# Performance work log

Measured on AMD Instinct MI355X. Metric: run time of the kernel, lower is better.

## Reference

```python
import jax, jax.numpy as jnp
import numpy as np

B, S, D, H = 4, 2048, 1024, 64  # batch, chunk_size, token_emb_dim, head_size

def setup_inputs() -> dict:
    key = jax.random.key(0)
    ks = jax.random.split(key, 6)
    sc = 0.02
    return {
        "x": jax.random.normal(ks[0], (B, S, D), dtype=jnp.float32),
        "Wq": jax.random.normal(ks[1], (D, H), dtype=jnp.float32) * sc,
        "Wk": jax.random.normal(ks[2], (D, H), dtype=jnp.float32) * sc,
        "Wv": jax.random.normal(ks[3], (D, H), dtype=jnp.float32) * sc,
        "Wproj": jax.random.normal(ks[4], (D, D), dtype=jnp.float32) * sc,
        "bproj": jax.random.normal(ks[5], (D,), dtype=jnp.float32) * sc,
        "n_heads": 16,
    }

def reference(x, Wq, Wk, Wv, Wproj, bproj, n_heads):
    # NOTE: the original torch module reuses ONE head instance n_heads times,
    # so every head produces the identical output. Compute once, tile.
    q = jnp.einsum('bsd,dh->bsh', x, Wq)
    k = jnp.einsum('bsd,dh->bsh', x, Wk)
    v = jnp.einsum('bsd,dh->bsh', x, Wv)
    scores = jnp.einsum('bqh,bkh->bqk', q, k) * (H ** -0.5)
    causal = jnp.tril(jnp.ones((S, S), dtype=bool))
    scores = jnp.where(causal[None, :, :], scores, -jnp.inf)
    attn = jax.nn.softmax(scores, axis=-1)
    ctx = jnp.einsum('bqk,bkh->bqh', attn, v)       # [B,S,H]
    out = jnp.tile(ctx, (1, 1, n_heads))            # concat of identical heads -> [B,S,D]
    return jnp.einsum('bsd,de->bse', out, Wproj) + bproj
```

## Files before the change

### kernel.cpp

```cpp
#include <hip/hip_runtime.h>
#include <hip/hip_bf16.h>
#include <math.h>

namespace {

constexpr int B = 4, S = 2048, D = 1024, H = 64, NH = 16;
constexpr int BS = B * S;
constexpr float SCALE2 = 0.125f * 1.4426950408889634f;
constexpr float M0 = 8.0f;

constexpr int AUNITS_PB = 272;
constexpr int AUNITS = AUNITS_PB * 4;

using f32x4 = __attribute__((ext_vector_type(4))) float;
using short8b = __attribute__((ext_vector_type(8))) short;

__device__ inline ushort f2bf(float f) {
    __hip_bfloat16 h = __float2bfloat16(f);
    return *reinterpret_cast<ushort*>(&h);
}
__device__ inline float bf2f(ushort u) {
    __hip_bfloat16 h = *reinterpret_cast<__hip_bfloat16*>(&u);
    return __bfloat162float(h);
}
__device__ inline int cum_units(int J) {
    return (J & 1) ? ((J + 1) * (J + 1) / 4) : (J * J / 4 + J / 2);
}

__global__ __launch_bounds__(256) void prep_kernel(const float* __restrict__ Wq,
                                                   const float* __restrict__ Wk,
                                                   const float* __restrict__ Wv,
                                                   const float* __restrict__ Wproj,
                                                   ushort* __restrict__ Wt,
                                                   ushort* __restrict__ Wpet) {
    const int bid = blockIdx.x;
    const int tid = threadIdx.x;
    if (bid < 768) {
        const int idx = bid * 256 + tid;
        const int n = idx >> 10, k = idx & 1023;
        const float* __restrict__ W = (n < 64) ? Wq : (n < 128) ? Wk : Wv;
        Wt[idx] = f2bf(W[k * 64 + (n & 63)]);
    } else {
        const int idx = (bid - 768) * 256 + tid;
        const int e = idx & 1023, h = idx >> 10;
        float s = 0.f;
#pragma unroll
        for (int t = 0; t < NH; ++t) s += Wproj[(t * H + h) * D + e];
        Wpet[e * 64 + h] = f2bf(s);
    }
}

__global__ __launch_bounds__(256) void qkv6_kernel(const float* __restrict__ x,
                                                   const ushort* __restrict__ Wt,
                                                   ushort* __restrict__ qb,
                                                   ushort* __restrict__ kb,
                                                   ushort* __restrict__ vb) {
    __shared__ ushort xs[16 * 128];
    __shared__ ushort wsm[192 * 128];
    const int tid = threadIdx.x;
    const int lane = tid & 63;
    const int li = lane & 15, lg = lane >> 4;
    const int wn = tid >> 6;
    const int row0 = blockIdx.x * 16;

    f32x4 acc[3];
#pragma unroll
    for (int t = 0; t < 3; ++t) acc[t] = (f32x4){0.f, 0.f, 0.f, 0.f};

    const int xrow = tid >> 4;
    const int xc4 = (tid & 15) * 4;

    const char* xsb = reinterpret_cast<const char*>(xs);
    const char* wsb = reinterpret_cast<const char*>(wsm);

    for (int k0 = 0; k0 < 1024; k0 += 128) {
        __syncthreads();
#pragma unroll
        for (int hh = 0; hh < 2; ++hh) {
            const float4 f = *reinterpret_cast<const float4*>(
                x + (size_t)(row0 + xrow) * 1024 + k0 + hh * 64 + xc4);
            ushort u[4] = {f2bf(f.x), f2bf(f.y), f2bf(f.z), f2bf(f.w)};
            int boff = xrow * 256 + (hh * 64 + xc4) * 2;
            boff ^= (xrow & 7) << 4;
            *reinterpret_cast<uint2*>(const_cast<char*>(xsb) + boff) =
                *reinterpret_cast<uint2*>(u);
        }
#pragma unroll
        for (int it = 0; it < 12; ++it) {
            const int cid = tid + it * 256;
            const int n = cid >> 4, kc = cid & 15;
            const int4 val = *reinterpret_cast<const int4*>(
                Wt + (size_t)n * 1024 + k0 + kc * 8);
            int boff = n * 256 + kc * 16;
            boff ^= (n & 7) << 4;
            *reinterpret_cast<int4*>(const_cast<char*>(wsb) + boff) = val;
        }
        __syncthreads();

        short8b a[4];
#pragma unroll
        for (int c2 = 0; c2 < 4; ++c2) {
            int aoff = li * 256 + c2 * 64 + lg * 16;
            aoff ^= (li & 7) << 4;
            a[c2] = *reinterpret_cast<const short8b*>(xsb + aoff);
        }
#pragma unroll
        for (int t = 0; t < 3; ++t) {
            const int n = wn * 48 + t * 16 + li;
            const int swz = (n & 7) << 4;
#pragma unroll
            for (int c2 = 0; c2 < 4; ++c2) {
                int boff = (n * 256 + c2 * 64 + lg * 16) ^ swz;
                const short8b bfrag = *reinterpret_cast<const short8b*>(wsb + boff);
                acc[t] = __builtin_amdgcn_mfma_f32_16x16x32_bf16(a[c2], bfrag, acc[t], 0, 0, 0);
            }
        }
    }

#pragma unroll
    for (int t = 0; t < 3; ++t) {
        const int col = wn * 48 + t * 16 + li;
        const int m = col >> 6, cc = col & 63;
        ushort* __restrict__ dst = (m == 0) ? qb : (m == 1) ? kb : vb;
        const float sc = (m == 0) ? SCALE2 : 1.f;
#pragma unroll
        for (int r = 0; r < 4; ++r) {
            const int gr = row0 + lg * 4 + r;
            dst[(size_t)gr * 64 + cc] = f2bf(acc[t][r] * sc);
        }
    }
}

__global__ __launch_bounds__(256) void attn_mfma3_kernel(const ushort* __restrict__ qb,
                                                         const ushort* __restrict__ kb16,
                                                         const ushort* __restrict__ vb16,
                                                         ushort* __restrict__ po,
                                                         float* __restrict__ pl) {
    __shared__ ushort ksm[64 * 64];
    __shared__ ushort vtm[64 * 64];
    __shared__ ushort plds[4][16 * 72];

    const int tid = threadIdx.x;
    const int lane = tid & 63;
    const int wave = tid >> 6;
    const int li = lane & 15, lg = lane >> 4;
    const int u = blockIdx.x;
    const int b = u & 3;
    const int ub = u >> 2;

    int J = (int)(2.f * sqrtf((float)ub + 0.5f));
    if (J > 31) J = 31;
    while (cum_units(J + 1) <= ub) ++J;
    while (cum_units(J) > ub) --J;
    const int c = ub - cum_units(J);
    const int kt_begin = 2 * c;
    const int kt_end = min(2 * c + 2, J + 1);

    const ushort* qg = qb + (size_t)(b * S + J * 64 + wave * 16 + li) * 64 + lg * 8;
    const short8b aq0 = *reinterpret_cast<const short8b*>(qg);
    const short8b aq1 = *reinterpret_cast<const short8b*>(qg + 32);

    short8b bones;
#pragma unroll
    for (int i = 0; i < 8; ++i) bones[i] = (short)0x3F80;

    f32x4 oacc[4];
#pragma unroll
    for (int t = 0; t < 4; ++t) oacc[t] = (f32x4){0.f, 0.f, 0.f, 0.f};
    f32x4 lacc = (f32x4){0.f, 0.f, 0.f, 0.f};

    for (int kt = kt_begin; kt < kt_end; ++kt) {
        __syncthreads();
        {
            const ushort* kg = kb16 + (size_t)(b * S + kt * 64) * 64;
#pragma unroll
            for (int it = 0; it < 2; ++it) {
                const int f = tid + it * 256;
                const int key = f >> 3, hd8 = f & 7;
                const int4 val = *reinterpret_cast<const int4*>(kg + key * 64 + hd8 * 8);
                int byteoff = (key << 7) + (hd8 << 4);
                byteoff ^= (key & 7) << 4;
                *reinterpret_cast<int4*>(reinterpret_cast<char*>(ksm) + byteoff) = val;
            }
        }
        {
            const ushort* vg = vb16 + (size_t)(b * S + kt * 64) * 64;
            const int kk = tid >> 4;
            const int hq = tid & 15;
            const uint2 a0 = *reinterpret_cast<const uint2*>(vg + (kk * 4 + 0) * 64 + hq * 4);
            const uint2 a1 = *reinterpret_cast<const uint2*>(vg + (kk * 4 + 1) * 64 + hq * 4);
            const uint2 a2 = *reinterpret_cast<const uint2*>(vg + (kk * 4 + 2) * 64 + hq * 4);
            const uint2 a3 = *reinterpret_cast<const uint2*>(vg + (kk * 4 + 3) * 64 + hq * 4);
#pragma unroll
            for (int i = 0; i < 4; ++i) {
                const uint s0 = (i < 2) ? a0.x : a0.y;
                const uint s1 = (i < 2) ? a1.x : a1.y;
                const uint s2 = (i < 2) ? a2.x : a2.y;
                const uint s3 = (i < 2) ? a3.x : a3.y;
                const uint sel = (i & 1) ? 0x07060302u : 0x05040100u;
                const uint w0 = __builtin_amdgcn_perm(s1, s0, sel);
                const uint w1 = __builtin_amdgcn_perm(s3, s2, sel);
                const int h = hq * 4 + i;
                int byteoff = (h << 7) + (kk << 3);
                byteoff ^= (h & 7) << 4;
                *reinterpret_cast<uint2*>(reinterpret_cast<char*>(vtm) + byteoff) =
                    make_uint2(w0, w1);
            }
        }
        __syncthreads();

        f32x4 accs[4];
#pragma unroll
        for (int t = 0; t < 4; ++t) accs[t] = (f32x4){0.f, 0.f, 0.f, 0.f};
#pragma unroll
        for (int t = 0; t < 4; ++t) {
            const int key = t * 16 + li;
#pragma unroll
            for (int c2 = 0; c2 < 2; ++c2) {
                int byteoff = (key << 7) + (c2 << 6) + (lg << 4);
                byteoff ^= (key & 7) << 4;
                const short8b bk = *reinterpret_cast<const short8b*>(
                    reinterpret_cast<const char*>(ksm) + byteoff);
                accs[t] = __builtin_amdgcn_mfma_f32_16x16x32_bf16(
                    (c2 == 0) ? aq0 : aq1, bk, accs[t], 0, 0, 0);
            }
        }

        const bool straddle = (kt == J);
#pragma unroll
        for (int t = 0; t < 4; ++t) {
            const int kg2 = kt * 64 + t * 16 + li;
#pragma unroll
            for (int r = 0; r < 4; ++r) {
                const int qrow = J * 64 + wave * 16 + lg * 4 + r;
                const float s = (straddle && kg2 > qrow) ? -1e30f : accs[t][r];
                plds[wave][(lg * 4 + r) * 72 + t * 16 + li] = f2bf(exp2f(s - M0));
            }
        }

        const short8b ap0 = *reinterpret_cast<const short8b*>(
            reinterpret_cast<const char*>(plds[wave]) + li * 144 + (lg << 4));
        const short8b ap1 = *reinterpret_cast<const short8b*>(
            reinterpret_cast<const char*>(plds[wave]) + li * 144 + 64 + (lg << 4));
#pragma unroll
        for (int t = 0; t < 4; ++t) {
            const int h = t * 16 + li;
#pragma unroll
            for (int c2 = 0; c2 < 2; ++c2) {
                int byteoff = (h << 7) + (c2 << 6) + (lg << 4);
                byteoff ^= (h & 7) << 4;
                const short8b bv = *reinterpret_cast<const short8b*>(
                    reinterpret_cast<const char*>(vtm) + byteoff);
                oacc[t] = __builtin_amdgcn_mfma_f32_16x16x32_bf16(
                    (c2 == 0) ? ap0 : ap1, bv, oacc[t], 0, 0, 0);
            }
        }
        lacc = __builtin_amdgcn_mfma_f32_16x16x32_bf16(ap0, bones, lacc, 0, 0, 0);
        lacc = __builtin_amdgcn_mfma_f32_16x16x32_bf16(ap1, bones, lacc, 0, 0, 0);
    }

    if (li == 0) {
#pragma unroll
        for (int r = 0; r < 4; ++r)
            pl[u * 64 + wave * 16 + lg * 4 + r] = lacc[r];
    }
#pragma unroll
    for (int t = 0; t < 4; ++t)
#pragma unroll
        for (int r = 0; r < 4; ++r)
            po[(size_t)u * 4096 + (wave * 16 + lg * 4 + r) * 64 + t * 16 + li] =
                f2bf(oacc[t][r]);
}

__global__ __launch_bounds__(256) void proj_fused_kernel(const ushort* __restrict__ po,
                                                         const float* __restrict__ pl,
                                                         const ushort* __restrict__ Wpet,
                                                         const float* __restrict__ bias,
                                                         float* __restrict__ out) {
    __shared__ ushort ctxs[16 * 64];
    const int tid = threadIdx.x;
    const int bid = blockIdx.x;
    const int b = bid >> 7, j = bid & 127;
    const int J = j >> 2;
    const int nc = (J + 2) >> 1;
    const int cumJ = cum_units(J);

    {
        const int qr = tid >> 4, hq = tid & 15;
        const int riu = (j & 3) * 16 + qr;
        float denom = 0.f;
        float acc[4] = {0.f, 0.f, 0.f, 0.f};
        for (int cc = 0; cc < nc; ++cc) {
            const int uu = (cumJ + cc) * 4 + b;
            denom += pl[uu * 64 + riu];
            const ushort* pp = po + (size_t)uu * 4096 + riu * 64 + hq * 4;
            acc[0] += bf2f(pp[0]);
            acc[1] += bf2f(pp[1]);
            acc[2] += bf2f(pp[2]);
            acc[3] += bf2f(pp[3]);
        }
        const float inv = 1.f / denom;
        ushort uu4[4] = {f2bf(acc[0] * inv), f2bf(acc[1] * inv),
                         f2bf(acc[2] * inv), f2bf(acc[3] * inv)};
        int boff = qr * 128 + hq * 8;
        boff ^= (qr & 7) << 4;
        *reinterpret_cast<uint2*>(reinterpret_cast<char*>(ctxs) + boff) =
            *reinterpret_cast<uint2*>(uu4);
    }
    __syncthreads();

    const int lane = tid & 63;
    const int li = lane & 15, lg = lane >> 4;
    const int wave = tid >> 6;
    const int col0 = wave * 256;
    const int row0 = bid * 16;

    int aoff = li * 128 + lg * 16;
    aoff ^= (li & 7) << 4;
    const short8b a0 = *reinterpret_cast<const short8b*>(
        reinterpret_cast<const char*>(ctxs) + aoff);
    const short8b a1 = *reinterpret_cast<const short8b*>(
        reinterpret_cast<const char*>(ctxs) + (aoff ^ 64));

#pragma unroll
    for (int t = 0; t < 16; ++t) {
        const int col = col0 + t * 16 + li;
        const ushort* bg = Wpet + (size_t)col * 64 + lg * 8;
        const short8b b0 = *reinterpret_cast<const short8b*>(bg);
        const short8b b1 = *reinterpret_cast<const short8b*>(bg + 32);
        f32x4 acc = (f32x4){0.f, 0.f, 0.f, 0.f};
        acc = __builtin_amdgcn_mfma_f32_16x16x32_bf16(a0, b0, acc, 0, 0, 0);
        acc = __builtin_amdgcn_mfma_f32_16x16x32_bf16(a1, b1, acc, 0, 0, 0);
        const float bb = bias[col];
#pragma unroll
        for (int r = 0; r < 4; ++r)
            out[(size_t)(row0 + lg * 4 + r) * 1024 + col] = acc[r] + bb;
    }
}

}

extern "C" void kernel_launch(void* const* d_in, const int* in_sizes, int n_in,
                              void* d_out, int out_size, void* d_ws, size_t ws_size,
                              hipStream_t stream) {
    const float* x     = (const float*)d_in[0];
    const float* Wq    = (const float*)d_in[1];
    const float* Wk    = (const float*)d_in[2];
    const float* Wv    = (const float*)d_in[3];
    const float* Wproj = (const float*)d_in[4];
    const float* bproj = (const float*)d_in[5];
    float* out = (float*)d_out;

    const size_t BSH = (size_t)BS * H;
    ushort* qb   = (ushort*)d_ws;
    ushort* kb   = qb + BSH;
    ushort* vb   = kb + BSH;
    ushort* Wt   = vb + BSH;
    ushort* Wpet = Wt + 192 * 1024;
    ushort* po   = Wpet + 65536;
    float*  pl   = (float*)(po + (size_t)AUNITS * 4096);

    hipLaunchKernelGGL(prep_kernel, dim3(1024), dim3(256), 0, stream, Wq, Wk, Wv, Wproj, Wt, Wpet);
    hipLaunchKernelGGL(qkv6_kernel, dim3(BS / 16), dim3(256), 0, stream, x, Wt, qb, kb, vb);
    hipLaunchKernelGGL(attn_mfma3_kernel, dim3(AUNITS), dim3(256), 0, stream,
                       qb, kb, vb, po, pl);
    hipLaunchKernelGGL(proj_fused_kernel, dim3(512), dim3(256), 0, stream,
                       po, pl, Wpet, bproj, out);
}
```

Measured before the change: 54.31 us.

## Process full 128-key tile per attention work unit in one pass

The attention kernel stops looping over two 64-key tiles with a pair of barriers per tile. It now loads a 128-key block of K and transposed V into enlarged shared memory in one go, syncs once, and computes all eight QK^T score tiles before two P·V halves. This removes the per-tile barrier and serialized load/compute phases and exposes more independent MFMA work. In exchange it uses more LDS and registers, which may lower occupancy. It also always applies the causal mask and does a full 128-key load even for the trailing single-tile units, where the extra 64 keys are fully masked.

```diff
diff --git a/kernel.cpp b/kernel.cpp
--- a/kernel.cpp
+++ b/kernel.cpp
@@ -131,14 +131,14 @@
     }
 }
 
-__global__ __launch_bounds__(256) void attn_mfma3_kernel(const ushort* __restrict__ qb,
+__global__ __launch_bounds__(256) void attn_mfma4_kernel(const ushort* __restrict__ qb,
                                                          const ushort* __restrict__ kb16,
                                                          const ushort* __restrict__ vb16,
                                                          ushort* __restrict__ po,
                                                          float* __restrict__ pl) {
-    __shared__ ushort ksm[64 * 64];
-    __shared__ ushort vtm[64 * 64];
-    __shared__ ushort plds[4][16 * 72];
+    __shared__ ushort ksm[128 * 64];
+    __shared__ ushort vtm[64 * 128];
+    __shared__ ushort plds[4][2][16 * 72];
 
     const int tid = threadIdx.x;
     const int lane = tid & 63;
@@ -153,8 +153,7 @@
     while (cum_units(J + 1) <= ub) ++J;
     while (cum_units(J) > ub) --J;
     const int c = ub - cum_units(J);
-    const int kt_begin = 2 * c;
-    const int kt_end = min(2 * c + 2, J + 1);
+    const int key0 = c * 128;
 
     const ushort* qg = qb + (size_t)(b * S + J * 64 + wave * 16 + li) * 64 + lg * 8;
     const short8b aq0 = *reinterpret_cast<const short8b*>(qg);
@@ -164,29 +163,25 @@
 #pragma unroll
     for (int i = 0; i < 8; ++i) bones[i] = (short)0x3F80;
 
-    f32x4 oacc[4];
-#pragma unroll
-    for (int t = 0; t < 4; ++t) oacc[t] = (f32x4){0.f, 0.f, 0.f, 0.f};
-    f32x4 lacc = (f32x4){0.f, 0.f, 0.f, 0.f};
-
-    for (int kt = kt_begin; kt < kt_end; ++kt) {
-        __syncthreads();
-        {
-            const ushort* kg = kb16 + (size_t)(b * S + kt * 64) * 64;
-#pragma unroll
-            for (int it = 0; it < 2; ++it) {
-                const int f = tid + it * 256;
-                const int key = f >> 3, hd8 = f & 7;
-                const int4 val = *reinterpret_cast<const int4*>(kg + key * 64 + hd8 * 8);
-                int byteoff = (key << 7) + (hd8 << 4);
-                byteoff ^= (key & 7) << 4;
-                *reinterpret_cast<int4*>(reinterpret_cast<char*>(ksm) + byteoff) = val;
-            }
-        }
-        {
-            const ushort* vg = vb16 + (size_t)(b * S + kt * 64) * 64;
-            const int kk = tid >> 4;
-            const int hq = tid & 15;
+    {
+        const ushort* kg = kb16 + (size_t)(b * S + key0) * 64;
+#pragma unroll
+        for (int it = 0; it < 4; ++it) {
+            const int f = tid + it * 256;
+            const int key = f >> 3, hd8 = f & 7;
+            const int4 val = *reinterpret_cast<const int4*>(kg + key * 64 + hd8 * 8);
+            int byteoff = (key << 7) + (hd8 << 4);
+            byteoff ^= (key & 7) << 4;
+            *reinterpret_cast<int4*>(reinterpret_cast<char*>(ksm) + byteoff) = val;
+        }
+    }
+    {
+        const ushort* vg = vb16 + (size_t)(b * S + key0) * 64;
+#pragma unroll
+        for (int it = 0; it < 2; ++it) {
+            const int item = tid + it * 256;
+            const int kk = item >> 4;
+            const int hq = item & 15;
             const uint2 a0 = *reinterpret_cast<const uint2*>(vg + (kk * 4 + 0) * 64 + hq * 4);
             const uint2 a1 = *reinterpret_cast<const uint2*>(vg + (kk * 4 + 1) * 64 + hq * 4);
             const uint2 a2 = *reinterpret_cast<const uint2*>(vg + (kk * 4 + 2) * 64 + hq * 4);
@@ -201,53 +196,60 @@
                 const uint w0 = __builtin_amdgcn_perm(s1, s0, sel);
                 const uint w1 = __builtin_amdgcn_perm(s3, s2, sel);
                 const int h = hq * 4 + i;
-                int byteoff = (h << 7) + (kk << 3);
+                int byteoff = (h << 8) + (kk << 3);
                 byteoff ^= (h & 7) << 4;
                 *reinterpret_cast<uint2*>(reinterpret_cast<char*>(vtm) + byteoff) =
                     make_uint2(w0, w1);
             }
         }
-        __syncthreads();
-
-        f32x4 accs[4];
-#pragma unroll
-        for (int t = 0; t < 4; ++t) accs[t] = (f32x4){0.f, 0.f, 0.f, 0.f};
-#pragma unroll
-        for (int t = 0; t < 4; ++t) {
-            const int key = t * 16 + li;
-#pragma unroll
-            for (int c2 = 0; c2 < 2; ++c2) {
-                int byteoff = (key << 7) + (c2 << 6) + (lg << 4);
-                byteoff ^= (key & 7) << 4;
-                const short8b bk = *reinterpret_cast<const short8b*>(
-                    reinterpret_cast<const char*>(ksm) + byteoff);
-                accs[t] = __builtin_amdgcn_mfma_f32_16x16x32_bf16(
-                    (c2 == 0) ? aq0 : aq1, bk, accs[t], 0, 0, 0);
-            }
-        }
-
-        const bool straddle = (kt == J);
-#pragma unroll
-        for (int t = 0; t < 4; ++t) {
-            const int kg2 = kt * 64 + t * 16 + li;
+    }
+    __syncthreads();
+
+    f32x4 accs[8];
+#pragma unroll
+    for (int t = 0; t < 8; ++t) accs[t] = (f32x4){0.f, 0.f, 0.f, 0.f};
+#pragma unroll
+    for (int t = 0; t < 8; ++t) {
+        const int key = t * 16 + li;
+#pragma unroll
+        for (int c2 = 0; c2 < 2; ++c2) {
+            int byteoff = (key << 7) + (c2 << 6) + (lg << 4);
+            byteoff ^= (key & 7) << 4;
+            const short8b bk = *reinterpret_cast<const short8b*>(
+                reinterpret_cast<const char*>(ksm) + byteoff);
+            accs[t] = __builtin_amdgcn_mfma_f32_16x16x32_bf16(
+                (c2 == 0) ? aq0 : aq1, bk, accs[t], 0, 0, 0);
+        }
+    }
+
+    f32x4 oacc[4];
+#pragma unroll
+    for (int t = 0; t < 4; ++t) oacc[t] = (f32x4){0.f, 0.f, 0.f, 0.f};
+    f32x4 lacc = (f32x4){0.f, 0.f, 0.f, 0.f};
+
+#pragma unroll
+    for (int half = 0; half < 2; ++half) {
+#pragma unroll
+        for (int tt = 0; tt < 4; ++tt) {
+            const int t = half * 4 + tt;
+            const int key = key0 + t * 16 + li;
 #pragma unroll
             for (int r = 0; r < 4; ++r) {
                 const int qrow = J * 64 + wave * 16 + lg * 4 + r;
-                const float s = (straddle && kg2 > qrow) ? -1e30f : accs[t][r];
-                plds[wave][(lg * 4 + r) * 72 + t * 16 + li] = f2bf(exp2f(s - M0));
+                const float s = (key > qrow) ? -1e30f : accs[t][r];
+                plds[wave][half][(lg * 4 + r) * 72 + tt * 16 + li] = f2bf(exp2f(s - M0));
             }
         }
 
-        const short8b ap0 = *reinterpret_cast<const short8b*>(
-            reinterpret_cast<const char*>(plds[wave]) + li * 144 + (lg << 4));
-        const short8b ap1 = *reinterpret_cast<const short8b*>(
-            reinterpret_cast<const char*>(plds[wave]) + li * 144 + 64 + (lg << 4));
+        const char* pb = reinterpret_cast<const char*>(plds[wave][half]);
+        const short8b ap0 = *reinterpret_cast<const short8b*>(pb + li * 144 + (lg << 4));
+        const short8b ap1 = *reinterpret_cast<const short8b*>(pb + li * 144 + 64 + (lg << 4));
 #pragma unroll
         for (int t = 0; t < 4; ++t) {
             const int h = t * 16 + li;
 #pragma unroll
             for (int c2 = 0; c2 < 2; ++c2) {
-                int byteoff = (h << 7) + (c2 << 6) + (lg << 4);
+                int byteoff = (h << 8) + (half << 7) + (c2 << 6) + (lg << 4);
                 byteoff ^= (h & 7) << 4;
                 const short8b bv = *reinterpret_cast<const short8b*>(
                     reinterpret_cast<const char*>(vtm) + byteoff);
@@ -362,7 +364,7 @@
 
     hipLaunchKernelGGL(prep_kernel, dim3(1024), dim3(256), 0, stream, Wq, Wk, Wv, Wproj, Wt, Wpet);
     hipLaunchKernelGGL(qkv6_kernel, dim3(BS / 16), dim3(256), 0, stream, x, Wt, qb, kb, vb);
-    hipLaunchKernelGGL(attn_mfma3_kernel, dim3(AUNITS), dim3(256), 0, stream,
+    hipLaunchKernelGGL(attn_mfma4_kernel, dim3(AUNITS), dim3(256), 0, stream,
                        qb, kb, vb, po, pl);
     hipLaunchKernelGGL(proj_fused_kernel, dim3(512), dim3(256), 0, stream,
                        po, pl, Wpet, bproj, out);
```

New measurement: 53.47 us. Within noise of the previous version (-1.6%).
